# Performance work log

Hardware: AMD Instinct MI355X
Metric: run time of the kernel (lower is better)

## Reference

```python
import jax, jax.numpy as jnp
import numpy as np

L = 7          # num_gc_layers
H = 64         # hidden_channels
N = 100000     # nodes
E = 1000000    # edges
G = 512        # graphs in batch
ATOM_DIMS = [119, 5, 12, 12, 10, 6, 6, 2, 2]   # OGB full_atom_feature_dims
BOND_DIMS = [5, 6, 2]                          # OGB full_bond_feature_dims
EPS_GEN = 1e-7   # GENConv message eps
EPS_BN = 1e-5    # BatchNorm eps
ATOM_OFF = np.concatenate([[0], np.cumsum(ATOM_DIMS)[:-1]]).astype(np.int64)
BOND_OFF = np.concatenate([[0], np.cumsum(BOND_DIMS)[:-1]]).astype(np.int64)


def setup_inputs() -> dict:
    key = jax.random.key(0)
    ks = jax.random.split(key, 12)
    x = jax.random.randint(ks[0], (N, len(ATOM_DIMS)), 0, 2)
    edge_index = jax.random.randint(ks[1], (2, E), 0, N)
    edge_attr = jax.random.randint(ks[2], (E, len(BOND_DIMS)), 0, 2)
    batch = jnp.sort(jax.random.randint(ks[3], (N,), 0, G))
    s = 0.02
    w = 1.0 / np.sqrt(H).astype(np.float32)
    return {
        "atom_table": jax.random.normal(ks[4], (sum(ATOM_DIMS), H), jnp.float32) * s,
        "bond_table": jax.random.normal(ks[5], (sum(BOND_DIMS), H), jnp.float32) * s,
        "vn0": jnp.zeros((H,), jnp.float32),  # virtualnode embedding, const-init 0
        "gcn_W": jax.random.normal(ks[6], (L, H, H), jnp.float32) * w,
        "gcn_b": jnp.zeros((L, H), jnp.float32),
        "norm_gamma": jnp.ones((L, H), jnp.float32),
        "norm_beta": jnp.zeros((L, H), jnp.float32),
        "vn_W1": jax.random.normal(ks[7], (L - 1, H, H), jnp.float32) * w,
        "vn_b1": jnp.zeros((L - 1, H), jnp.float32),
        "vn_g1": jnp.ones((L - 1, H), jnp.float32),
        "vn_be1": jnp.zeros((L - 1, H), jnp.float32),
        "vn_W2": jax.random.normal(ks[8], (L - 1, H, H), jnp.float32) * w,
        "vn_b2": jnp.zeros((L - 1, H), jnp.float32),
        "vn_g2": jnp.ones((L - 1, H), jnp.float32),
        "vn_be2": jnp.zeros((L - 1, H), jnp.float32),
        "x": x,
        "edge_index": edge_index,
        "edge_attr": edge_attr,
        "batch": batch,
        "classification": 0,
    }


def _bn(h, g, b):
    # BatchNorm1d, training mode (biased batch stats over the node axis)
    mu = h.mean(0)
    var = h.var(0)
    return (h - mu) * jax.lax.rsqrt(var + EPS_BN) * g + b


def _genconv(h, src, dst, edge_emb, W, b):
    # GENConv, aggr='add', mlp_layers=1 (single last_lin Linear)
    msg = jax.nn.relu(h[src] + edge_emb) + EPS_GEN        # [E, H]
    m = jax.ops.segment_sum(msg, dst, num_segments=N)     # [N, H]
    return (h + m) @ W + b


def reference(atom_table, bond_table, vn0, gcn_W, gcn_b, norm_gamma, norm_beta,
              vn_W1, vn_b1, vn_g1, vn_be1, vn_W2, vn_b2, vn_g2, vn_be2,
              x, edge_index, edge_attr, batch, classification):
    # AtomEncoder / BondEncoder: sum of per-feature embeddings via offset table
    h = atom_table[x + jnp.asarray(ATOM_OFF)].sum(1)                   # [N, H]
    edge_emb = bond_table[edge_attr + jnp.asarray(BOND_OFF)].sum(1)    # [E, H]
    vn = jnp.broadcast_to(vn0[None, :], (G, H))                        # [G, H]
    h = h + vn[batch]
    src, dst = edge_index[0], edge_index[1]

    # block == 'res+': conv0, then [BN -> ReLU -> (vnode) -> conv -> +res]
    h = _genconv(h, src, dst, edge_emb, gcn_W[0], gcn_b[0])
    for l in range(1, L):
        h2 = jax.nn.relu(_bn(h, norm_gamma[l - 1], norm_beta[l - 1]))
        # virtual-node update: global_add_pool + 2-layer MLP (Lin-BN-ReLU x2)
        vt = jax.ops.segment_sum(h2, batch, num_segments=G) + vn
        z = jax.nn.relu(_bn(vt @ vn_W1[l - 1] + vn_b1[l - 1], vn_g1[l - 1], vn_be1[l - 1]))
        vn = jax.nn.relu(_bn(z @ vn_W2[l - 1] + vn_b2[l - 1], vn_g2[l - 1], vn_be2[l - 1]))
        h2 = h2 + vn[batch]
        h = _genconv(h2, src, dst, edge_emb, gcn_W[l], gcn_b[l]) + h
    h = _bn(h, norm_gamma[L - 1], norm_beta[L - 1])

    # classification=False -> global_mean_pool readout
    cnt = jax.ops.segment_sum(jnp.ones((N,), h.dtype), batch, num_segments=G)
    out = jax.ops.segment_sum(h, batch, num_segments=G) / jnp.clip(cnt, 1.0)[:, None]
    return out
```

## Files before the change

kernel.cpp:

```cpp
#include <hip/hip_runtime.h>
#include <hip/hip_bf16.h>
#include <hip/hip_fp16.h>

#define NN 100000
#define EE 1000000
#define GG 512
#define HH 64
#define LL 7
#define NH (NN*HH)
#define GH (GG*HH)
#define EPS_GEN 1e-7f
#define EPS_BN 1e-5f
#define SCAN_BLKS 98
#define SLOTS 64
#define CONV_BLOCKS 6250

typedef _Float16 half8  __attribute__((ext_vector_type(8)));
typedef _Float16 half4  __attribute__((ext_vector_type(4)));
typedef _Float16 half2v __attribute__((ext_vector_type(2)));
typedef float    float4v __attribute__((ext_vector_type(4)));

__device__ __constant__ int c_atom_off[9] = {0,119,124,136,148,158,164,170,172};

__global__ void k_atom_enc(const float* __restrict__ atom_table,
                           const float* __restrict__ vn0,
                           const int* __restrict__ x,
                           _Float16* __restrict__ h16) {
    int tid = blockIdx.x * blockDim.x + threadIdx.x;
    int n = tid >> 6, c = tid & 63;
    if (n >= NN) return;
    float acc = vn0[c];
    const int* xr = x + n * 9;
    #pragma unroll
    for (int f = 0; f < 9; ++f) acc += atom_table[(xr[f] + c_atom_off[f]) * HH + c];
    h16[tid] = (_Float16)acc;
}

__global__ void k_prep(const float* __restrict__ W, const float* __restrict__ bond,
                       _Float16* __restrict__ W16f, _Float16* __restrict__ ctab16) {
    int i = blockIdx.x * blockDim.x + threadIdx.x;
    if (i < LL * 4096) {
        int l = i / 4096, r = i % 4096;
        int j = r & 7, lane = (r >> 3) & 63, kh = (r >> 9) & 1, t = r >> 10;
        int q = (lane >> 4) & 3, c = lane & 15;
        W16f[i] = (_Float16)W[l * 4096 + (kh * 32 + q * 8 + j) * 64 + t * 16 + c];
    } else {
        int k = i - LL * 4096;
        if (k < 60 * 64) {
            int cmb = k >> 6, lane = k & 63;
            int a0 = cmb % 5, a1 = (cmb / 5) % 6, a2 = cmb / 30;
            ctab16[k] = (_Float16)(bond[a0 * 64 + lane] + bond[(5 + a1) * 64 + lane]
                                   + bond[(11 + a2) * 64 + lane]);
        }
    }
}

__global__ void k_count2(const int* __restrict__ edge_index, const int* __restrict__ edge_attr,
                         int* __restrict__ cur, unsigned int* __restrict__ recs) {
    int e = blockIdx.x * blockDim.x + threadIdx.x;
    if (e >= EE) return;
    int src = edge_index[e];
    int dst = edge_index[EE + e];
    int combo = edge_attr[e * 3] + 5 * edge_attr[e * 3 + 1] + 30 * edge_attr[e * 3 + 2];
    unsigned int rank = (unsigned int)atomicAdd(&cur[dst], 1);
    recs[e] = (unsigned int)src | ((unsigned int)combo << 17) | (rank << 23);
}

__global__ void k_scan1(const int* __restrict__ cnt, int* __restrict__ rp, int* __restrict__ part) {
    __shared__ int s[256];
    int t = threadIdx.x, blk = blockIdx.x;
    int base = blk * 1024 + t * 4;
    int v0 = 0, v1 = 0, v2 = 0, v3 = 0;
    if (base + 3 < NN) {
        int4 q = *(const int4*)(cnt + base);
        v0 = q.x; v1 = q.y; v2 = q.z; v3 = q.w;
    } else {
        if (base + 0 < NN) v0 = cnt[base + 0];
        if (base + 1 < NN) v1 = cnt[base + 1];
        if (base + 2 < NN) v2 = cnt[base + 2];
        if (base + 3 < NN) v3 = cnt[base + 3];
    }
    int s4 = v0 + v1 + v2 + v3;
    s[t] = s4;
    __syncthreads();
    for (int off = 1; off < 256; off <<= 1) {
        int x = (t >= off) ? s[t - off] : 0;
        __syncthreads();
        s[t] += x;
        __syncthreads();
    }
    int excl = s[t] - s4;
    if (t == 255) part[blk] = s[255];
    if (base + 0 < NN) rp[base + 0] = excl;
    if (base + 1 < NN) rp[base + 1] = excl + v0;
    if (base + 2 < NN) rp[base + 2] = excl + v0 + v1;
    if (base + 3 < NN) rp[base + 3] = excl + v0 + v1 + v2;
}

__global__ void k_scan2(int* __restrict__ part) {
    __shared__ int s[128];
    int t = threadIdx.x;
    int v = (t < SCAN_BLKS) ? part[t] : 0;
    s[t] = v;
    __syncthreads();
    for (int off = 1; off < 128; off <<= 1) {
        int x = (t >= off) ? s[t - off] : 0;
        __syncthreads();
        s[t] += x;
        __syncthreads();
    }
    if (t < SCAN_BLKS) part[t] = s[t] - v;
}

__global__ void k_scan3(int* __restrict__ rp, const int* __restrict__ part) {
    int i = blockIdx.x * blockDim.x + threadIdx.x;
    if (i < NN) rp[i] += part[i >> 10];
    if (i == 0) rp[NN] = EE;
}

__global__ void k_fill2(const int* __restrict__ edge_index, const unsigned int* __restrict__ recs,
                        const int* __restrict__ rp, unsigned int* __restrict__ edges) {
    int e = blockIdx.x * blockDim.x + threadIdx.x;
    if (e >= EE) return;
    unsigned int rec = recs[e];
    int dst = edge_index[EE + e];
    edges[rp[dst] + (rec >> 23)] = rec & 0x7FFFFFu;
}

__global__ __launch_bounds__(128, 8) void k_conv_mfma(
        const _Float16* __restrict__ h16, const float* res,
        const int* __restrict__ rp, const unsigned int* __restrict__ edges,
        const _Float16* __restrict__ ctab16, const _Float16* __restrict__ W16f,
        const float* __restrict__ bvec,
        float* __restrict__ out, float* __restrict__ statsPart) {
    __shared__ __align__(16) _Float16 sA[16 * 64];
    __shared__ __align__(16) _Float16 sC[60 * 64];
    int lane = threadIdx.x & 63;
    int wv = threadIdx.x >> 6;
    int g  = lane >> 5;
    int sg = (lane >> 4) & 1;
    int cc = (lane & 15) * 4;
    int q = lane >> 4;
    int c = lane & 15;
    int lane32 = lane & 31;
    int n0 = blockIdx.x * 16;
    const half4 z4 = {(_Float16)0, (_Float16)0, (_Float16)0, (_Float16)0};

    for (int i = threadIdx.x; i < 480; i += 128)
        ((int4*)sC)[i] = ((const int4*)ctab16)[i];

    const half8* wf = (const half8*)W16f;
    half8 bf[2][2];
    #pragma unroll
    for (int t = 0; t < 2; ++t) {
        bf[t][0] = wf[((wv * 2 + t) * 2 + 0) * 64 + lane];
        bf[t][1] = wf[((wv * 2 + t) * 2 + 1) * 64 + lane];
    }
    __syncthreads();

    #pragma unroll 1
    for (int i = 0; i < 4; ++i) {
        int r_loc = wv * 8 + g * 4 + i;
        int n = n0 + r_loc;
        int beg = rp[n], end = rp[n + 1];
        int deg = end - beg;
        half4 sv = *(const half4*)(h16 + (size_t)n * 64 + cc);
        float ax = 0.f, ay = 0.f, az = 0.f, aw = 0.f;
        #pragma unroll 1
        for (int base = beg; base < end; base += 32) {
            int idx = base + lane32;
            idx = idx < end ? idx : end - 1;
            unsigned int rl = edges[idx];
            int m = end - base; if (m > 32) m = 32;
            int t = 0;
            for (; t + 8 <= m; t += 8) {
                unsigned int r[4];
                #pragma unroll
                for (int u = 0; u < 4; ++u)
                    r[u] = __shfl(rl, (g << 5) + t + 2 * u + sg, 64);
                half4 hh[4], tt[4];
                #pragma unroll
                for (int u = 0; u < 4; ++u) {
                    hh[u] = *(const half4*)(h16 + (size_t)(r[u] & 0x1FFFF) * 64 + cc);
                    tt[u] = *(const half4*)(sC + ((r[u] >> 17) & 63) * 64 + cc);
                }
                #pragma unroll
                for (int u = 0; u < 4; ++u) {
                    half4 mm = __builtin_elementwise_max(hh[u] + tt[u], z4);
                    ax += (float)mm[0]; ay += (float)mm[1];
                    az += (float)mm[2]; aw += (float)mm[3];
                }
            }
            for (; t < m; t += 2) {
                int e0 = t + sg;
                bool v0 = e0 < m;
                unsigned int r0 = __shfl(rl, (g << 5) + (v0 ? e0 : 0), 64);
                half4 h0 = *(const half4*)(h16 + (size_t)(r0 & 0x1FFFF) * 64 + cc);
                half4 t0 = *(const half4*)(sC + ((r0 >> 17) & 63) * 64 + cc);
                half4 m0 = __builtin_elementwise_max(h0 + t0, z4);
                if (v0) {
                    ax += (float)m0[0]; ay += (float)m0[1];
                    az += (float)m0[2]; aw += (float)m0[3];
                }
            }
        }
        ax += __shfl_xor(ax, 16, 64); ay += __shfl_xor(ay, 16, 64);
        az += __shfl_xor(az, 16, 64); aw += __shfl_xor(aw, 16, 64);
        float ed = (float)deg * EPS_GEN;
        ax += (float)sv[0] + ed; ay += (float)sv[1] + ed;
        az += (float)sv[2] + ed; aw += (float)sv[3] + ed;
        if (sg == 0) {
            half4 pk;
            pk[0] = (_Float16)ax; pk[1] = (_Float16)ay;
            pk[2] = (_Float16)az; pk[3] = (_Float16)aw;
            *(half4*)(&sA[r_loc * 64 + cc]) = pk;
        }
    }
    __syncthreads();

    half8 af0 = *(const half8*)(sA + c * 64 + q * 8);
    half8 af1 = *(const half8*)(sA + c * 64 + 32 + q * 8);
    float4v d[2];
    #pragma unroll
    for (int t = 0; t < 2; ++t) {
        d[t] = (float4v){0.f, 0.f, 0.f, 0.f};
        d[t] = __builtin_amdgcn_mfma_f32_16x16x32_f16(af0, bf[t][0], d[t], 0, 0, 0);
        d[t] = __builtin_amdgcn_mfma_f32_16x16x32_f16(af1, bf[t][1], d[t], 0, 0, 0);
    }

    float ps[2], pq[2];
    #pragma unroll
    for (int t = 0; t < 2; ++t) { ps[t] = 0.f; pq[t] = 0.f; }
    #pragma unroll
    for (int t = 0; t < 2; ++t) {
        int tg = wv * 2 + t;
        float bz = bvec[tg * 16 + c];
        #pragma unroll
        for (int r = 0; r < 4; ++r) {
            int row = n0 + q * 4 + r;
            float val = d[t][r] + bz;
            size_t off = (size_t)row * 64 + tg * 16 + c;
            if (res) val += res[off];
            out[off] = val;
            ps[t] += val;
            pq[t] = fmaf(val, val, pq[t]);
        }
    }
    #pragma unroll
    for (int t = 0; t < 2; ++t) {
        ps[t] += __shfl_xor(ps[t], 16, 64); ps[t] += __shfl_xor(ps[t], 32, 64);
        pq[t] += __shfl_xor(pq[t], 16, 64); pq[t] += __shfl_xor(pq[t], 32, 64);
    }
    float* sp = statsPart + ((blockIdx.x * 2 + wv) & (SLOTS - 1)) * 128;
    if (lane < 16) {
        #pragma unroll
        for (int t = 0; t < 2; ++t) {
            int tg = wv * 2 + t;
            atomicAdd(&sp[tg * 16 + lane], ps[t]);
            atomicAdd(&sp[64 + tg * 16 + lane], pq[t]);
        }
    }
}


__global__ void k_bn_relu_vt2(const float* __restrict__ h, const float* __restrict__ spart,
                              const float* __restrict__ gamma, const float* __restrict__ beta,
                              const int* __restrict__ batch,
                              _Float16* __restrict__ h16, float* __restrict__ vt) {
    __shared__ float sTmp[256];
    __shared__ float sMS[128];
    {
        int ch = threadIdx.x & 127, hf = threadIdx.x >> 7;
        float a = 0.f;
        #pragma unroll 8
        for (int i = hf; i < SLOTS; i += 2) a += spart[i * 128 + ch];
        sTmp[threadIdx.x] = a;
    }
    __syncthreads();
    if (threadIdx.x < 64) {
        int c = threadIdx.x;
        float s = sTmp[c] + sTmp[128 + c];
        float q = sTmp[64 + c] + sTmp[192 + c];
        float mu = s * (1.f / NN);
        float var = q * (1.f / NN) - mu * mu;
        sMS[c] = mu;
        sMS[64 + c] = rsqrtf(var + EPS_BN);
    }
    __syncthreads();
    int lane = threadIdx.x & 63;
    int w = blockIdx.x * 4 + (threadIdx.x >> 6);
    int n0 = w * 8;
    if (n0 >= NN) return;
    int n1 = min(n0 + 8, NN);
    float mu = sMS[lane];
    float inv = sMS[64 + lane] * gamma[lane];
    float bet = beta[lane];
    float acc = 0.f;
    int gcur = batch[n0];
    for (int n = n0; n < n1; ++n) {
        float v = fmaxf((h[(size_t)n * 64 + lane] - mu) * inv + bet, 0.f);
        h16[(size_t)n * 64 + lane] = (_Float16)v;
        int g = batch[n];
        if (g != gcur) {
            atomicAdd(&vt[(size_t)gcur * 64 + lane], acc);
            acc = 0.f; gcur = g;
        }
        acc += v;
    }
    atomicAdd(&vt[(size_t)gcur * 64 + lane], acc);
}

__global__ void k_vn_gemm(float* __restrict__ in, int clear_in,
                          const float* in_stats, const float* in_g, const float* in_be,
                          const float* addmat, const float* add_stats,
                          const float* add_g, const float* add_be,
                          const float* addvec,
                          const float* __restrict__ W, const float* __restrict__ bvec,
                          float* __restrict__ out, float* __restrict__ out_stats) {
    __shared__ float sW[4096];
    __shared__ float sRed[2][4][64];
    for (int i = threadIdx.x; i < 4096; i += 256) sW[i] = W[i];
    __syncthreads();
    int lane = threadIdx.x & 63, wv = threadIdx.x >> 6;
    int w = blockIdx.x * 4 + wv;
    float imu = 0.f, iinv = 0.f, ibe = 0.f;
    if (in_stats) {
        float mu = in_stats[lane] * (1.f / GG);
        float var = in_stats[64 + lane] * (1.f / GG) - mu * mu;
        imu = mu; iinv = rsqrtf(var + EPS_BN) * in_g[lane]; ibe = in_be[lane];
    }
    float amu = 0.f, ainv = 0.f, abe = 0.f;
    if (addmat && add_stats) {
        float mu = add_stats[lane] * (1.f / GG);
        float var = add_stats[64 + lane] * (1.f / GG) - mu * mu;
        amu = mu; ainv = rsqrtf(var + EPS_BN) * add_g[lane]; abe = add_be[lane];
    }
    float av_const = addvec ? addvec[lane] : 0.f;
    float psum = 0.f, psq = 0.f;
    for (int r = w * 4; r < w * 4 + 4; ++r) {
        float va = in[r * 64 + lane];
        if (clear_in) in[r * 64 + lane] = 0.f;
        if (in_stats) va = fmaxf((va - imu) * iinv + ibe, 0.f);
        if (addmat) va += fmaxf((addmat[r * 64 + lane] - amu) * ainv + abe, 0.f);
        va += av_const;
        float acc = bvec[lane];
        #pragma unroll
        for (int k = 0; k < 64; ++k)
            acc = fmaf(__shfl(va, k, 64), sW[k * 64 + lane], acc);
        out[r * 64 + lane] = acc;
        psum += acc; psq = fmaf(acc, acc, psq);
    }
    sRed[0][wv][lane] = psum;
    sRed[1][wv][lane] = psq;
    __syncthreads();
    if (threadIdx.x < 64) {
        float s = 0.f, q = 0.f;
        #pragma unroll
        for (int i = 0; i < 4; ++i) { s += sRed[0][i][threadIdx.x]; q += sRed[1][i][threadIdx.x]; }
        atomicAdd(&out_stats[threadIdx.x], s);
        atomicAdd(&out_stats[64 + threadIdx.x], q);
    }
}

__global__ void k_addvn16(_Float16* __restrict__ h16, const float* __restrict__ t2,
                          const float* __restrict__ stats,
                          const float* __restrict__ g2, const float* __restrict__ be2,
                          const int* __restrict__ batch) {
    int tid = blockIdx.x * blockDim.x + threadIdx.x;
    int n = tid >> 4, p = tid & 15;
    if (n >= NN) return;
    int c0 = p * 4;
    float mu[4], iv[4], be[4];
    #pragma unroll
    for (int k = 0; k < 4; ++k) {
        int ci = c0 + k;
        float m = stats[ci] * (1.f / GG);
        float v = stats[64 + ci] * (1.f / GG) - m * m;
        mu[k] = m;
        iv[k] = rsqrtf(v + EPS_BN) * g2[ci];
        be[k] = be2[ci];
    }
    int g = batch[n];
    float4 t = *(const float4*)(t2 + (size_t)g * 64 + c0);
    float tv[4] = {t.x, t.y, t.z, t.w};
    half4 hv = *(half4*)(h16 + (size_t)n * 64 + c0);
    half4 o;
    #pragma unroll
    for (int k = 0; k < 4; ++k) {
        float a = fmaxf((tv[k] - mu[k]) * iv[k] + be[k], 0.f);
        o[k] = (_Float16)((float)hv[k] + a);
    }
    *(half4*)(h16 + (size_t)n * 64 + c0) = o;
}

__global__ void k_pool2(const float* __restrict__ h, const float* __restrict__ spart,
                        const float* __restrict__ gamma, const float* __restrict__ beta,
                        const int* __restrict__ batch,
                        float* __restrict__ out, float* __restrict__ cnt) {
    __shared__ float sTmp[256];
    __shared__ float sMS[128];
    {
        int ch = threadIdx.x & 127, hf = threadIdx.x >> 7;
        float a = 0.f;
        #pragma unroll 8
        for (int i = hf; i < SLOTS; i += 2) a += spart[i * 128 + ch];
        sTmp[threadIdx.x] = a;
    }
    __syncthreads();
    if (threadIdx.x < 64) {
        int c = threadIdx.x;
        float s = sTmp[c] + sTmp[128 + c];
        float q = sTmp[64 + c] + sTmp[192 + c];
        float mu = s * (1.f / NN);
        float var = q * (1.f / NN) - mu * mu;
        sMS[c] = mu;
        sMS[64 + c] = rsqrtf(var + EPS_BN);
    }
    __syncthreads();
    int lane = threadIdx.x & 63;
    int w = blockIdx.x * 4 + (threadIdx.x >> 6);
    int n0 = w * 16;
    if (n0 >= NN) return;
    int n1 = min(n0 + 16, NN);
    float mu = sMS[lane];
    float inv = sMS[64 + lane] * gamma[lane];
    float bet = beta[lane];
    float acc = 0.f;
    int run = 0;
    int gcur = batch[n0];
    for (int n = n0; n < n1; ++n) {
        float v = (h[(size_t)n * 64 + lane] - mu) * inv + bet;
        int g = batch[n];
        if (g != gcur) {
            atomicAdd(&out[(size_t)gcur * 64 + lane], acc);
            if (lane == 0) atomicAdd(&cnt[gcur], (float)run);
            acc = 0.f; run = 0; gcur = g;
        }
        acc += v; run++;
    }
    atomicAdd(&out[(size_t)gcur * 64 + lane], acc);
    if (lane == 0) atomicAdd(&cnt[gcur], (float)run);
}

__global__ void k_div(float* __restrict__ out, const float* __restrict__ cnt) {
    int tid = blockIdx.x * blockDim.x + threadIdx.x;
    if (tid >= GH) return;
    out[tid] /= fmaxf(cnt[tid >> 6], 1.0f);
}

extern "C" void kernel_launch(void* const* d_in, const int* in_sizes, int n_in,
                              void* d_out, int out_size, void* d_ws, size_t ws_size,
                              hipStream_t stream) {
    const float* atom_table = (const float*)d_in[0];
    const float* bond_table = (const float*)d_in[1];
    const float* vn0   = (const float*)d_in[2];
    const float* gcn_W = (const float*)d_in[3];
    const float* gcn_b = (const float*)d_in[4];
    const float* ng    = (const float*)d_in[5];
    const float* nb    = (const float*)d_in[6];
    const float* vn_W1 = (const float*)d_in[7];
    const float* vn_b1 = (const float*)d_in[8];
    const float* vn_g1 = (const float*)d_in[9];
    const float* vn_be1= (const float*)d_in[10];
    const float* vn_W2 = (const float*)d_in[11];
    const float* vn_b2 = (const float*)d_in[12];
    const float* vn_g2 = (const float*)d_in[13];
    const float* vn_be2= (const float*)d_in[14];
    const int* x          = (const int*)d_in[15];
    const int* edge_index = (const int*)d_in[16];
    const int* edge_attr  = (const int*)d_in[17];
    const int* batch      = (const int*)d_in[18];

    float* ws = (float*)d_ws;
    float* hB   = ws;
    _Float16* h16 = (_Float16*)(ws + (size_t)NH);
    float* vt   = ws + (size_t)NH + NH / 2;
    float* t1   = vt + GH;
    float* t2   = t1 + GH;
    float* convStatsP = t2 + GH;
    float* msAll      = convStatsP + 7 * SLOTS * 128;
    float* vn1Stats   = msAll + 7 * 128;
    float* vn2Stats   = vn1Stats + 6 * 128;
    float* cnt    = vn2Stats + 6 * 128;
    _Float16* ctab16 = (_Float16*)(cnt + GG);
    _Float16* W16f   = ctab16 + 60 * 64;
    int*   rp     = (int*)(W16f + LL * 4096);
    int*   cur    = rp + (NN + 2);
    int*   part   = cur + NN;
    unsigned int* edges = (unsigned int*)(part + 128);
    unsigned int* recs = (unsigned int*)h16;

    const int blkN = NH / 256;
    const int blkG = (GH + 255) / 256;
    const int blkE = (EE + 255) / 256;
    const int blkRL = ((NN + 7) / 8 + 3) / 4;
    const int blkPL = ((NN + 15) / 16 + 3) / 4;
    const int blkAV = (NN * 16) / 256;
    const int blkPR = (LL * 4096 + 60 * 64 + 255) / 256;
    float* outp = (float*)d_out;

    hipMemsetAsync(cur, 0, (size_t)NN * 4, stream);
    k_count2<<<blkE, 256, 0, stream>>>(edge_index, edge_attr, cur, recs);
    k_scan1<<<SCAN_BLKS, 256, 0, stream>>>(cur, rp, part);
    k_scan2<<<1, 128, 0, stream>>>(part);
    k_scan3<<<(NN + 255) / 256, 256, 0, stream>>>(rp, part);
    k_fill2<<<blkE, 256, 0, stream>>>(edge_index, recs, rp, edges);

    k_atom_enc<<<blkN, 256, 0, stream>>>(atom_table, vn0, x, h16);
    k_prep<<<blkPR, 256, 0, stream>>>(gcn_W, bond_table, W16f, ctab16);
    hipMemsetAsync(convStatsP, 0, (7 * SLOTS * 128 + 7 * 128 + 12 * 128) * 4, stream);
    hipMemsetAsync(vt, 0, (size_t)GH * 4, stream);

    k_conv_mfma<<<CONV_BLOCKS, 128, 0, stream>>>(h16, nullptr, rp, edges, ctab16, W16f,
                                                 gcn_b, hB, convStatsP);

    for (int l = 1; l < LL; ++l) {
        k_bn_relu_vt2<<<blkRL, 256, 0, stream>>>(hB, convStatsP + (size_t)(l - 1) * SLOTS * 128,
                                                 ng + (size_t)(l - 1) * HH,
                                                 nb + (size_t)(l - 1) * HH, batch, h16, vt);
        if (l == 1)
            k_vn_gemm<<<32, 256, 0, stream>>>(vt, 1, nullptr, nullptr, nullptr,
                                              nullptr, nullptr, nullptr, nullptr, vn0,
                                              vn_W1, vn_b1, t1, vn1Stats);
        else
            k_vn_gemm<<<32, 256, 0, stream>>>(vt, 1, nullptr, nullptr, nullptr,
                                              t2, vn2Stats + (size_t)(l - 2) * 128,
                                              vn_g2 + (size_t)(l - 2) * HH,
                                              vn_be2 + (size_t)(l - 2) * HH, nullptr,
                                              vn_W1 + (size_t)(l - 1) * 4096,
                                              vn_b1 + (size_t)(l - 1) * HH, t1,
                                              vn1Stats + (size_t)(l - 1) * 128);
        k_vn_gemm<<<32, 256, 0, stream>>>(t1, 0, vn1Stats + (size_t)(l - 1) * 128,
                                          vn_g1 + (size_t)(l - 1) * HH,
                                          vn_be1 + (size_t)(l - 1) * HH,
                                          nullptr, nullptr, nullptr, nullptr, nullptr,
                                          vn_W2 + (size_t)(l - 1) * 4096,
                                          vn_b2 + (size_t)(l - 1) * HH, t2,
                                          vn2Stats + (size_t)(l - 1) * 128);
        k_addvn16<<<blkAV, 256, 0, stream>>>(h16, t2, vn2Stats + (size_t)(l - 1) * 128,
                                             vn_g2 + (size_t)(l - 1) * HH,
                                             vn_be2 + (size_t)(l - 1) * HH, batch);

        k_conv_mfma<<<CONV_BLOCKS, 128, 0, stream>>>(h16, hB, rp, edges, ctab16,
                                                     W16f + (size_t)l * 4096,
                                                     gcn_b + (size_t)l * HH, hB,
                                                     convStatsP + (size_t)l * SLOTS * 128);
    }

    hipMemsetAsync(outp, 0, (size_t)GH * 4, stream);
    hipMemsetAsync(cnt, 0, (size_t)GG * 4, stream);
    k_pool2<<<blkPL, 256, 0, stream>>>(hB, convStatsP + (size_t)6 * SLOTS * 128,
                                       ng + (size_t)6 * HH, nb + (size_t)6 * HH,
                                       batch, outp, cnt);
    k_div<<<blkG, 256, 0, stream>>>(outp, cnt);
}
```

Baseline: 781.2 us.

## Fuse virtual-node MLP into one block and pack degree counters into bytes

The two per-layer virtual-node GEMM launches (32 blocks each, with global atomics for BN stats) are merged into a single 512-thread, single-block kernel. It computes both linear layers, takes the intermediate BatchNorm statistics in shared memory, and writes the final stats directly instead of through atomics. This removes a launch and an atomic round-trip per layer, but runs the MLP on one CU. Separately, in-degree counters are packed four per 32-bit word so the count atomics and the scan read less memory. This assumes no node has more than 255 incoming edges, or the packed counts overflow into the neighbouring node.

```diff
diff --git a/kernel.cpp b/kernel.cpp
--- a/kernel.cpp
+++ b/kernel.cpp
@@ -56,30 +56,26 @@
 }
 
 __global__ void k_count2(const int* __restrict__ edge_index, const int* __restrict__ edge_attr,
-                         int* __restrict__ cur, unsigned int* __restrict__ recs) {
+                         unsigned int* __restrict__ cur, unsigned int* __restrict__ recs) {
     int e = blockIdx.x * blockDim.x + threadIdx.x;
     if (e >= EE) return;
     int src = edge_index[e];
     int dst = edge_index[EE + e];
     int combo = edge_attr[e * 3] + 5 * edge_attr[e * 3 + 1] + 30 * edge_attr[e * 3 + 2];
-    unsigned int rank = (unsigned int)atomicAdd(&cur[dst], 1);
+    int sh = (dst & 3) * 8;
+    unsigned int old = atomicAdd(&cur[dst >> 2], 1u << sh);
+    unsigned int rank = (old >> sh) & 255u;
     recs[e] = (unsigned int)src | ((unsigned int)combo << 17) | (rank << 23);
 }
 
-__global__ void k_scan1(const int* __restrict__ cnt, int* __restrict__ rp, int* __restrict__ part) {
+__global__ void k_scan1(const unsigned int* __restrict__ cnt, int* __restrict__ rp,
+                        int* __restrict__ part) {
     __shared__ int s[256];
     int t = threadIdx.x, blk = blockIdx.x;
+    int wi = blk * 256 + t;
+    unsigned int pw = (wi < NN / 4) ? cnt[wi] : 0u;
+    int v0 = pw & 255, v1 = (pw >> 8) & 255, v2 = (pw >> 16) & 255, v3 = (pw >> 24) & 255;
     int base = blk * 1024 + t * 4;
-    int v0 = 0, v1 = 0, v2 = 0, v3 = 0;
-    if (base + 3 < NN) {
-        int4 q = *(const int4*)(cnt + base);
-        v0 = q.x; v1 = q.y; v2 = q.z; v3 = q.w;
-    } else {
-        if (base + 0 < NN) v0 = cnt[base + 0];
-        if (base + 1 < NN) v1 = cnt[base + 1];
-        if (base + 2 < NN) v2 = cnt[base + 2];
-        if (base + 3 < NN) v3 = cnt[base + 3];
-    }
     int s4 = v0 + v1 + v2 + v3;
     s[t] = s4;
     __syncthreads();
@@ -310,55 +306,84 @@
     atomicAdd(&vt[(size_t)gcur * 64 + lane], acc);
 }
 
-__global__ void k_vn_gemm(float* __restrict__ in, int clear_in,
-                          const float* in_stats, const float* in_g, const float* in_be,
-                          const float* addmat, const float* add_stats,
-                          const float* add_g, const float* add_be,
-                          const float* addvec,
-                          const float* __restrict__ W, const float* __restrict__ bvec,
-                          float* __restrict__ out, float* __restrict__ out_stats) {
-    __shared__ float sW[4096];
-    __shared__ float sRed[2][4][64];
-    for (int i = threadIdx.x; i < 4096; i += 256) sW[i] = W[i];
-    __syncthreads();
+__global__ __launch_bounds__(512, 1) void k_vn_mlp(
+        float* __restrict__ in,
+        const float* addmat, const float* add_stats,
+        const float* add_g, const float* add_be,
+        const float* addvec,
+        const float* __restrict__ W1, const float* __restrict__ b1,
+        const float* __restrict__ g1, const float* __restrict__ be1,
+        const float* __restrict__ W2, const float* __restrict__ b2,
+        float* __restrict__ t1g, float* t2,
+        float* __restrict__ t2stats) {
+    __shared__ float sW1[4096];
+    __shared__ float sW2[4096];
+    __shared__ float sRed[2][8][64];
+    for (int i = threadIdx.x; i < 4096; i += 512) { sW1[i] = W1[i]; sW2[i] = W2[i]; }
     int lane = threadIdx.x & 63, wv = threadIdx.x >> 6;
-    int w = blockIdx.x * 4 + wv;
-    float imu = 0.f, iinv = 0.f, ibe = 0.f;
-    if (in_stats) {
-        float mu = in_stats[lane] * (1.f / GG);
-        float var = in_stats[64 + lane] * (1.f / GG) - mu * mu;
-        imu = mu; iinv = rsqrtf(var + EPS_BN) * in_g[lane]; ibe = in_be[lane];
-    }
     float amu = 0.f, ainv = 0.f, abe = 0.f;
-    if (addmat && add_stats) {
+    if (addmat) {
         float mu = add_stats[lane] * (1.f / GG);
         float var = add_stats[64 + lane] * (1.f / GG) - mu * mu;
         amu = mu; ainv = rsqrtf(var + EPS_BN) * add_g[lane]; abe = add_be[lane];
     }
-    float av_const = addvec ? addvec[lane] : 0.f;
-    float psum = 0.f, psq = 0.f;
-    for (int r = w * 4; r < w * 4 + 4; ++r) {
+    float av = addvec ? addvec[lane] : 0.f;
+    float b1l = b1[lane], g1l = g1[lane], be1l = be1[lane], b2l = b2[lane];
+    __syncthreads();
+    int r0 = wv * 64;
+    float ps = 0.f, pq = 0.f;
+    #pragma unroll 1
+    for (int r = r0; r < r0 + 64; ++r) {
         float va = in[r * 64 + lane];
-        if (clear_in) in[r * 64 + lane] = 0.f;
-        if (in_stats) va = fmaxf((va - imu) * iinv + ibe, 0.f);
+        in[r * 64 + lane] = 0.f;
         if (addmat) va += fmaxf((addmat[r * 64 + lane] - amu) * ainv + abe, 0.f);
-        va += av_const;
-        float acc = bvec[lane];
+        va += av;
+        float a0 = b1l, a1 = 0.f;
         #pragma unroll
-        for (int k = 0; k < 64; ++k)
-            acc = fmaf(__shfl(va, k, 64), sW[k * 64 + lane], acc);
-        out[r * 64 + lane] = acc;
-        psum += acc; psq = fmaf(acc, acc, psq);
-    }
-    sRed[0][wv][lane] = psum;
-    sRed[1][wv][lane] = psq;
+        for (int k = 0; k < 64; k += 2) {
+            a0 = fmaf(__shfl(va, k, 64), sW1[k * 64 + lane], a0);
+            a1 = fmaf(__shfl(va, k + 1, 64), sW1[(k + 1) * 64 + lane], a1);
+        }
+        float acc = a0 + a1;
+        t1g[r * 64 + lane] = acc;
+        ps += acc; pq = fmaf(acc, acc, pq);
+    }
+    sRed[0][wv][lane] = ps;
+    sRed[1][wv][lane] = pq;
+    __syncthreads();
+    float s = 0.f, q = 0.f;
+    #pragma unroll
+    for (int i = 0; i < 8; ++i) { s += sRed[0][i][lane]; q += sRed[1][i][lane]; }
+    float mu1 = s * (1.f / GG);
+    float var1 = q * (1.f / GG) - mu1 * mu1;
+    float inv1 = rsqrtf(var1 + EPS_BN) * g1l;
+    float ps2 = 0.f, pq2 = 0.f;
+    #pragma unroll 1
+    for (int r = r0; r < r0 + 64; ++r) {
+        float va = fmaxf((t1g[r * 64 + lane] - mu1) * inv1 + be1l, 0.f);
+        float a0 = b2l, a1 = 0.f;
+        #pragma unroll
+        for (int k = 0; k < 64; k += 2) {
+            a0 = fmaf(__shfl(va, k, 64), sW2[k * 64 + lane], a0);
+            a1 = fmaf(__shfl(va, k + 1, 64), sW2[(k + 1) * 64 + lane], a1);
+        }
+        float acc = a0 + a1;
+        t2[r * 64 + lane] = acc;
+        ps2 += acc; pq2 = fmaf(acc, acc, pq2);
+    }
+    __syncthreads();
+    sRed[0][wv][lane] = ps2;
+    sRed[1][wv][lane] = pq2;
     __syncthreads();
     if (threadIdx.x < 64) {
-        float s = 0.f, q = 0.f;
+        float s2 = 0.f, q2 = 0.f;
         #pragma unroll
-        for (int i = 0; i < 4; ++i) { s += sRed[0][i][threadIdx.x]; q += sRed[1][i][threadIdx.x]; }
-        atomicAdd(&out_stats[threadIdx.x], s);
-        atomicAdd(&out_stats[64 + threadIdx.x], q);
+        for (int i = 0; i < 8; ++i) {
+            s2 += sRed[0][i][threadIdx.x];
+            q2 += sRed[1][i][threadIdx.x];
+        }
+        t2stats[threadIdx.x] = s2;
+        t2stats[64 + threadIdx.x] = q2;
     }
 }
 
@@ -499,9 +524,9 @@
     const int blkPR = (LL * 4096 + 60 * 64 + 255) / 256;
     float* outp = (float*)d_out;
 
-    hipMemsetAsync(cur, 0, (size_t)NN * 4, stream);
-    k_count2<<<blkE, 256, 0, stream>>>(edge_index, edge_attr, cur, recs);
-    k_scan1<<<SCAN_BLKS, 256, 0, stream>>>(cur, rp, part);
+    hipMemsetAsync(cur, 0, (size_t)(NN / 4) * 4, stream);
+    k_count2<<<blkE, 256, 0, stream>>>(edge_index, edge_attr, (unsigned int*)cur, recs);
+    k_scan1<<<SCAN_BLKS, 256, 0, stream>>>((const unsigned int*)cur, rp, part);
     k_scan2<<<1, 128, 0, stream>>>(part);
     k_scan3<<<(NN + 255) / 256, 256, 0, stream>>>(rp, part);
     k_fill2<<<blkE, 256, 0, stream>>>(edge_index, recs, rp, edges);
@@ -519,24 +544,20 @@
                                                  ng + (size_t)(l - 1) * HH,
                                                  nb + (size_t)(l - 1) * HH, batch, h16, vt);
         if (l == 1)
-            k_vn_gemm<<<32, 256, 0, stream>>>(vt, 1, nullptr, nullptr, nullptr,
-                                              nullptr, nullptr, nullptr, nullptr, vn0,
-                                              vn_W1, vn_b1, t1, vn1Stats);
+            k_vn_mlp<<<1, 512, 0, stream>>>(vt, nullptr, nullptr, nullptr, nullptr, vn0,
+                                            vn_W1, vn_b1, vn_g1, vn_be1,
+                                            vn_W2, vn_b2, t1, t2, vn2Stats);
         else
-            k_vn_gemm<<<32, 256, 0, stream>>>(vt, 1, nullptr, nullptr, nullptr,
-                                              t2, vn2Stats + (size_t)(l - 2) * 128,
-                                              vn_g2 + (size_t)(l - 2) * HH,
-                                              vn_be2 + (size_t)(l - 2) * HH, nullptr,
-                                              vn_W1 + (size_t)(l - 1) * 4096,
-                                              vn_b1 + (size_t)(l - 1) * HH, t1,
-                                              vn1Stats + (size_t)(l - 1) * 128);
-        k_vn_gemm<<<32, 256, 0, stream>>>(t1, 0, vn1Stats + (size_t)(l - 1) * 128,
-                                          vn_g1 + (size_t)(l - 1) * HH,
-                                          vn_be1 + (size_t)(l - 1) * HH,
-                                          nullptr, nullptr, nullptr, nullptr, nullptr,
-                                          vn_W2 + (size_t)(l - 1) * 4096,
-                                          vn_b2 + (size_t)(l - 1) * HH, t2,
-                                          vn2Stats + (size_t)(l - 1) * 128);
+            k_vn_mlp<<<1, 512, 0, stream>>>(vt, t2, vn2Stats + (size_t)(l - 2) * 128,
+                                            vn_g2 + (size_t)(l - 2) * HH,
+                                            vn_be2 + (size_t)(l - 2) * HH, nullptr,
+                                            vn_W1 + (size_t)(l - 1) * 4096,
+                                            vn_b1 + (size_t)(l - 1) * HH,
+                                            vn_g1 + (size_t)(l - 1) * HH,
+                                            vn_be1 + (size_t)(l - 1) * HH,
+                                            vn_W2 + (size_t)(l - 1) * 4096,
+                                            vn_b2 + (size_t)(l - 1) * HH,
+                                            t1, t2, vn2Stats + (size_t)(l - 1) * 128);
         k_addvn16<<<blkAV, 256, 0, stream>>>(h16, t2, vn2Stats + (size_t)(l - 1) * 128,
                                              vn_g2 + (size_t)(l - 1) * HH,
                                              vn_be2 + (size_t)(l - 1) * HH, batch);
```

New measurement: 1.706 ms. 118% more time.

## Gather 16-byte half8 rows per lane in conv, fold scan2 into scan3

Applied to the files above, without the earlier changes.

The conv gather loop now has each lane load 8 fp16 channels (half8) per edge instead of 4, so 4 edges are processed in parallel per 32-lane group, with a two-step xor-shuffle reduction at the end. This is meant to cut instruction count and make each gather load wider. The tail loop is merged into a predicated 16-edge step. The W fragment loads move after the gather to lower register pressure during it. The separate k_scan2 launch is removed: each k_scan3 block now sums the preceding partials itself, which saves a kernel launch at the cost of some redundant reduction work.

```diff
diff --git a/kernel.cpp b/kernel.cpp
--- a/kernel.cpp
+++ b/kernel.cpp
@@ -97,24 +97,18 @@
     if (base + 3 < NN) rp[base + 3] = excl + v0 + v1 + v2;
 }
 
-__global__ void k_scan2(int* __restrict__ part) {
-    __shared__ int s[128];
-    int t = threadIdx.x;
-    int v = (t < SCAN_BLKS) ? part[t] : 0;
-    s[t] = v;
-    __syncthreads();
-    for (int off = 1; off < 128; off <<= 1) {
-        int x = (t >= off) ? s[t - off] : 0;
+__global__ void k_scan3(int* __restrict__ rp, const int* __restrict__ part) {
+    __shared__ int s[256];
+    int p = blockIdx.x >> 2;
+    s[threadIdx.x] = (threadIdx.x < p) ? part[threadIdx.x] : 0;
+    __syncthreads();
+    for (int off = 128; off > 0; off >>= 1) {
+        if (threadIdx.x < off) s[threadIdx.x] += s[threadIdx.x + off];
         __syncthreads();
-        s[t] += x;
-        __syncthreads();
-    }
-    if (t < SCAN_BLKS) part[t] = s[t] - v;
-}
-
-__global__ void k_scan3(int* __restrict__ rp, const int* __restrict__ part) {
-    int i = blockIdx.x * blockDim.x + threadIdx.x;
-    if (i < NN) rp[i] += part[i >> 10];
+    }
+    int pre = s[0];
+    int i = blockIdx.x * 256 + threadIdx.x;
+    if (i < NN) rp[i] += pre;
     if (i == 0) rp[NN] = EE;
 }
 
@@ -138,24 +132,17 @@
     int lane = threadIdx.x & 63;
     int wv = threadIdx.x >> 6;
     int g  = lane >> 5;
-    int sg = (lane >> 4) & 1;
-    int cc = (lane & 15) * 4;
+    int lane32 = lane & 31;
+    int e_idx = lane32 >> 3;
+    int ch8 = (lane32 & 7) * 8;
     int q = lane >> 4;
     int c = lane & 15;
-    int lane32 = lane & 31;
     int n0 = blockIdx.x * 16;
-    const half4 z4 = {(_Float16)0, (_Float16)0, (_Float16)0, (_Float16)0};
+    const half8 z8 = {(_Float16)0, (_Float16)0, (_Float16)0, (_Float16)0,
+                      (_Float16)0, (_Float16)0, (_Float16)0, (_Float16)0};
 
     for (int i = threadIdx.x; i < 480; i += 128)
         ((int4*)sC)[i] = ((const int4*)ctab16)[i];
-
-    const half8* wf = (const half8*)W16f;
-    half8 bf[2][2];
-    #pragma unroll
-    for (int t = 0; t < 2; ++t) {
-        bf[t][0] = wf[((wv * 2 + t) * 2 + 0) * 64 + lane];
-        bf[t][1] = wf[((wv * 2 + t) * 2 + 1) * 64 + lane];
-    }
     __syncthreads();
 
     #pragma unroll 1
@@ -164,57 +151,61 @@
         int n = n0 + r_loc;
         int beg = rp[n], end = rp[n + 1];
         int deg = end - beg;
-        half4 sv = *(const half4*)(h16 + (size_t)n * 64 + cc);
-        float ax = 0.f, ay = 0.f, az = 0.f, aw = 0.f;
+        float acc[8];
+        #pragma unroll
+        for (int j = 0; j < 8; ++j) acc[j] = 0.f;
         #pragma unroll 1
         for (int base = beg; base < end; base += 32) {
             int idx = base + lane32;
             idx = idx < end ? idx : end - 1;
             unsigned int rl = edges[idx];
             int m = end - base; if (m > 32) m = 32;
-            int t = 0;
-            for (; t + 8 <= m; t += 8) {
+            #pragma unroll 1
+            for (int t = 0; t < m; t += 16) {
                 unsigned int r[4];
+                bool vld[4];
                 #pragma unroll
-                for (int u = 0; u < 4; ++u)
-                    r[u] = __shfl(rl, (g << 5) + t + 2 * u + sg, 64);
-                half4 hh[4], tt[4];
+                for (int k = 0; k < 4; ++k) {
+                    int e = t + k * 4 + e_idx;
+                    vld[k] = e < m;
+                    r[k] = __shfl(rl, (g << 5) + (vld[k] ? e : 0), 64);
+                }
+                half8 hh[4], tt[4];
                 #pragma unroll
-                for (int u = 0; u < 4; ++u) {
-                    hh[u] = *(const half4*)(h16 + (size_t)(r[u] & 0x1FFFF) * 64 + cc);
-                    tt[u] = *(const half4*)(sC + ((r[u] >> 17) & 63) * 64 + cc);
+                for (int k = 0; k < 4; ++k) {
+                    hh[k] = *(const half8*)(h16 + (size_t)(r[k] & 0x1FFFF) * 64 + ch8);
+                    tt[k] = *(const half8*)(sC + ((r[k] >> 17) & 63) * 64 + ch8);
                 }
                 #pragma unroll
-                for (int u = 0; u < 4; ++u) {
-                    half4 mm = __builtin_elementwise_max(hh[u] + tt[u], z4);
-                    ax += (float)mm[0]; ay += (float)mm[1];
-                    az += (float)mm[2]; aw += (float)mm[3];
+                for (int k = 0; k < 4; ++k) {
+                    half8 mm = __builtin_elementwise_max(hh[k] + tt[k], z8);
+                    if (vld[k]) {
+                        #pragma unroll
+                        for (int j = 0; j < 8; ++j) acc[j] += (float)mm[j];
+                    }
                 }
             }
-            for (; t < m; t += 2) {
-                int e0 = t + sg;
-                bool v0 = e0 < m;
-                unsigned int r0 = __shfl(rl, (g << 5) + (v0 ? e0 : 0), 64);
-                half4 h0 = *(const half4*)(h16 + (size_t)(r0 & 0x1FFFF) * 64 + cc);
-                half4 t0 = *(const half4*)(sC + ((r0 >> 17) & 63) * 64 + cc);
-                half4 m0 = __builtin_elementwise_max(h0 + t0, z4);
-                if (v0) {
-                    ax += (float)m0[0]; ay += (float)m0[1];
-                    az += (float)m0[2]; aw += (float)m0[3];
-                }
-            }
-        }
-        ax += __shfl_xor(ax, 16, 64); ay += __shfl_xor(ay, 16, 64);
-        az += __shfl_xor(az, 16, 64); aw += __shfl_xor(aw, 16, 64);
+        }
+        #pragma unroll
+        for (int j = 0; j < 8; ++j) {
+            acc[j] += __shfl_xor(acc[j], 8, 64);
+            acc[j] += __shfl_xor(acc[j], 16, 64);
+        }
+        half8 sv = *(const half8*)(h16 + (size_t)n * 64 + ch8);
         float ed = (float)deg * EPS_GEN;
-        ax += (float)sv[0] + ed; ay += (float)sv[1] + ed;
-        az += (float)sv[2] + ed; aw += (float)sv[3] + ed;
-        if (sg == 0) {
-            half4 pk;
-            pk[0] = (_Float16)ax; pk[1] = (_Float16)ay;
-            pk[2] = (_Float16)az; pk[3] = (_Float16)aw;
-            *(half4*)(&sA[r_loc * 64 + cc]) = pk;
-        }
+        half8 pk;
+        #pragma unroll
+        for (int j = 0; j < 8; ++j) pk[j] = (_Float16)(acc[j] + (float)sv[j] + ed);
+        if (e_idx == 0)
+            *(half8*)(&sA[r_loc * 64 + ch8]) = pk;
+    }
+
+    const half8* wf = (const half8*)W16f;
+    half8 bf[2][2];
+    #pragma unroll
+    for (int t = 0; t < 2; ++t) {
+        bf[t][0] = wf[((wv * 2 + t) * 2 + 0) * 64 + lane];
+        bf[t][1] = wf[((wv * 2 + t) * 2 + 1) * 64 + lane];
     }
     __syncthreads();
 
@@ -502,7 +493,6 @@
     hipMemsetAsync(cur, 0, (size_t)NN * 4, stream);
     k_count2<<<blkE, 256, 0, stream>>>(edge_index, edge_attr, cur, recs);
     k_scan1<<<SCAN_BLKS, 256, 0, stream>>>(cur, rp, part);
-    k_scan2<<<1, 128, 0, stream>>>(part);
     k_scan3<<<(NN + 255) / 256, 256, 0, stream>>>(rp, part);
     k_fill2<<<blkE, 256, 0, stream>>>(edge_index, recs, rp, edges);
 
```

Result: faster. 761.5 us (-2.5%).
